# Performance work log

Measured on AMD Instinct MI355X. Metric: run time of the kernel, lower is better.

## Reference

```python
import jax, jax.numpy as jnp
import numpy as np

N = 50000      # nodes (single 'paper' node type)
E = 800000     # edges per etype
ET = 3         # edge types
L = 3          # GAT layers (1 + num_hidden=2)
H = 4          # heads
DH = 64        # per-head dim (n_hidden // n_heads)
NH = H * DH    # 256
NC = 16        # classes
NEG_SLOPE = 0.2


def setup_inputs() -> dict:
    key = jax.random.key(0)
    ks = jax.random.split(key, 8)
    x = jax.random.normal(ks[0], (N, NH), jnp.float32)
    src = jax.random.randint(ks[1], (ET, E), 0, N, jnp.int32)
    dst = jax.random.randint(ks[2], (ET, E), 0, N, jnp.int32)
    W = jax.random.normal(ks[3], (L, ET, NH, NH), jnp.float32) * 0.05
    attn_l = jax.random.normal(ks[4], (L, ET, H, DH), jnp.float32) * 0.05
    attn_r = jax.random.normal(ks[5], (L, ET, H, DH), jnp.float32) * 0.05
    bias = jnp.zeros((L, ET, NH), jnp.float32)
    lin_w = jax.random.normal(ks[6], (NH, NC), jnp.float32) * 0.05
    lin_b = jnp.zeros((NC,), jnp.float32)
    return {"x": x, "src": src, "dst": dst, "W": W, "attn_l": attn_l,
            "attn_r": attn_r, "bias": bias, "lin_w": lin_w, "lin_b": lin_b}


def _gat(h, W_e, al, ar, b, s, d):
    # h: [N, NH] -> z: [N, H, DH]
    z = (h @ W_e).reshape(N, H, DH)
    el = jnp.sum(z * al, axis=-1)             # [N, H]  (src-side score)
    er = jnp.sum(z * ar, axis=-1)             # [N, H]  (dst-side score)
    e = jax.nn.leaky_relu(el[s] + er[d], NEG_SLOPE)   # [E, H]
    # edge softmax over incoming edges of each dst node
    m = jax.ops.segment_max(e, d, num_segments=N)     # [N, H]
    a = jnp.exp(e - m[d])                              # [E, H]
    denom = jax.ops.segment_sum(a, d, num_segments=N) # [N, H]
    alpha = a / denom[d]                               # [E, H]
    # weighted aggregation of source features
    out = jax.ops.segment_sum(alpha[:, :, None] * z[s], d, num_segments=N)  # [N, H, DH]
    return out.reshape(N, NH) + b


def reference(x, src, dst, W, attn_l, attn_r, bias, lin_w, lin_b):
    h = x
    for l in range(L):
        acc = jnp.zeros((N, NH), h.dtype)
        for t in range(ET):  # HeteroGraphConv 'sum' aggregation across etypes
            acc = acc + _gat(h, W[l, t], attn_l[l, t], attn_r[l, t],
                             bias[l, t], src[t], dst[t])
        h = acc
        if l != L - 1:
            h = jax.nn.relu(h)  # dropout is identity in eval
    return h @ lin_w + lin_b    # [N, NC]
```

## Files before the change

kernel.cpp:

```cpp
#include <hip/hip_runtime.h>
#include <hip/hip_bf16.h>
#include <math.h>

#define N_NODES 50000
#define NEDGE 800000
#define NET 3
#define LAYERS 3
#define HEADS 4
#define DHEAD 64
#define NH 256
#define NC 16
#define NEG_SLOPE 0.2f
#define MPAD 50048

typedef __attribute__((ext_vector_type(8))) short short8;
typedef __attribute__((ext_vector_type(4))) float f32x4;
typedef __attribute__((ext_vector_type(8))) _Float16 half8;

#define GLDS16(gp, lp) \
  __builtin_amdgcn_global_load_lds((const __attribute__((address_space(1))) void*)(gp), \
                                   (__attribute__((address_space(3))) void*)(lp), 16, 0, 0)

__device__ inline unsigned short f2bf(float x) {
  unsigned u = __float_as_uint(x);
  unsigned r = (u + 0x7FFFu + ((u >> 16) & 1u)) >> 16;
  return (unsigned short)r;
}
__device__ inline float bf2f(unsigned short h) { return __uint_as_float(((unsigned)h) << 16); }

__global__ void split_transpose_W(const float* __restrict__ W,
                                  unsigned short* __restrict__ WhT,
                                  unsigned short* __restrict__ WlT) {
  int i = blockIdx.x * blockDim.x + threadIdx.x;
  if (i >= LAYERS * NET * NH * NH) return;
  int mat = i >> 16, rem = i & 65535;
  int n = rem >> 8, k = rem & 255;
  float v = W[(size_t)mat * 65536 + k * 256 + n];
  unsigned short hi = f2bf(v);
  unsigned short lo = f2bf(v - bf2f(hi));
  WhT[(size_t)mat * 65536 + n * 256 + k] = hi;
  WlT[(size_t)mat * 65536 + n * 256 + k] = lo;
}

__global__ void split_kernel(const float* __restrict__ in, unsigned short* __restrict__ hi,
                             unsigned short* __restrict__ lo) {
  int i = blockIdx.x * blockDim.x + threadIdx.x;
  if (i >= N_NODES * NH / 4) return;
  float4 v = ((const float4*)in)[i];
  ushort4 h, l;
  h.x = f2bf(v.x); l.x = f2bf(v.x - bf2f(h.x));
  h.y = f2bf(v.y); l.y = f2bf(v.y - bf2f(h.y));
  h.z = f2bf(v.z); l.z = f2bf(v.z - bf2f(h.z));
  h.w = f2bf(v.w); l.w = f2bf(v.w - bf2f(h.w));
  ((ushort4*)hi)[i] = h;
  ((ushort4*)lo)[i] = l;
}

__global__ __launch_bounds__(256) void gemm_split(const unsigned short* __restrict__ Ah,
                                                  const unsigned short* __restrict__ Al,
                                                  const unsigned short* __restrict__ BhT,
                                                  const unsigned short* __restrict__ BlT,
                                                  const float* __restrict__ al,
                                                  const float* __restrict__ ar,
                                                  _Float16* __restrict__ zh,
                                                  float* __restrict__ el,
                                                  float* __restrict__ er, int M) {
  __shared__ unsigned short lds[20480];
  unsigned short* sAh = lds;
  unsigned short* sAl = lds + 2048;
  unsigned short* sBh = lds + 4096;
  unsigned short* sBl = lds + 12288;

  int tid = threadIdx.x;
  int w = tid >> 6, lane = tid & 63;
  int r16 = lane & 15, rk = lane >> 4;
  int bm = blockIdx.x * 64;

  int arow = tid >> 2, acol = (tid & 3) * 8;
  const unsigned short* pAh = Ah + (size_t)(bm + arow) * 256 + acol;
  const unsigned short* pAl = Al + (size_t)(bm + arow) * 256 + acol;

  f32x4 acc[4][4];
#pragma unroll
  for (int m = 0; m < 4; m++)
#pragma unroll
    for (int n = 0; n < 4; n++) acc[m][n] = (f32x4){0.f, 0.f, 0.f, 0.f};

  char* aldsA = (char*)lds + (size_t)w * 1024;

#pragma unroll
  for (int k0 = 0; k0 < 8; k0++) {
    GLDS16(pAh + k0 * 32, aldsA);
    GLDS16(pAl + k0 * 32, (char*)sAl + (size_t)w * 1024);
#pragma unroll
    for (int i = 0; i < 4; i++) {
      int slot = tid + i * 256;
      int nrow = slot >> 2, kcol = (slot & 3) * 8;
      size_t go = (size_t)nrow * 256 + k0 * 32 + kcol;
      char* lb = (char*)sBh + ((size_t)w * 64 + (size_t)i * 256) * 16;
      char* lb2 = (char*)sBl + ((size_t)w * 64 + (size_t)i * 256) * 16;
      GLDS16(BhT + go, lb);
      GLDS16(BlT + go, lb2);
    }
    __syncthreads();

    short8 a_h[4], a_l[4], b_h[4], b_l[4];
#pragma unroll
    for (int m = 0; m < 4; m++) {
      a_h[m] = *(const short8*)&sAh[(m * 16 + r16) * 32 + rk * 8];
      a_l[m] = *(const short8*)&sAl[(m * 16 + r16) * 32 + rk * 8];
    }
#pragma unroll
    for (int n = 0; n < 4; n++) {
      int col = w * 64 + n * 16 + r16;
      b_h[n] = *(const short8*)&sBh[col * 32 + rk * 8];
      b_l[n] = *(const short8*)&sBl[col * 32 + rk * 8];
    }
#pragma unroll
    for (int m = 0; m < 4; m++)
#pragma unroll
      for (int n = 0; n < 4; n++) {
        acc[m][n] = __builtin_amdgcn_mfma_f32_16x16x32_bf16(a_h[m], b_h[n], acc[m][n], 0, 0, 0);
        acc[m][n] = __builtin_amdgcn_mfma_f32_16x16x32_bf16(a_h[m], b_l[n], acc[m][n], 0, 0, 0);
        acc[m][n] = __builtin_amdgcn_mfma_f32_16x16x32_bf16(a_l[m], b_h[n], acc[m][n], 0, 0, 0);
      }
    __syncthreads();
  }

#pragma unroll
  for (int m = 0; m < 4; m++) {
    int row0 = bm + m * 16 + rk * 4;
#pragma unroll
    for (int n = 0; n < 4; n++) {
      int col = w * 64 + n * 16 + r16;
#pragma unroll
      for (int r = 0; r < 4; r++) {
        int row = row0 + r;
        if (row < M) zh[(size_t)row * 256 + col] = (_Float16)acc[m][n][r];
      }
    }
  }

  float alv[4], arv[4];
#pragma unroll
  for (int n = 0; n < 4; n++) {
    alv[n] = al[w * 64 + n * 16 + r16];
    arv[n] = ar[w * 64 + n * 16 + r16];
  }
#pragma unroll
  for (int m = 0; m < 4; m++) {
#pragma unroll
    for (int r = 0; r < 4; r++) {
      float pl = 0.f, pr = 0.f;
#pragma unroll
      for (int n = 0; n < 4; n++) {
        float zv = acc[m][n][r];
        pl = fmaf(zv, alv[n], pl);
        pr = fmaf(zv, arv[n], pr);
      }
      pl += __shfl_xor(pl, 1, 64); pl += __shfl_xor(pl, 2, 64);
      pl += __shfl_xor(pl, 4, 64); pl += __shfl_xor(pl, 8, 64);
      pr += __shfl_xor(pr, 1, 64); pr += __shfl_xor(pr, 2, 64);
      pr += __shfl_xor(pr, 4, 64); pr += __shfl_xor(pr, 8, 64);
      int row = bm + m * 16 + rk * 4 + r;
      if (r16 == 0 && row < M) {
        el[row * HEADS + w] = pl;
        er[row * HEADS + w] = pr;
      }
    }
  }
}

__device__ inline float leaky(float v) { return v > 0.f ? v : NEG_SLOPE * v; }

__global__ void deg_kernel(const int* __restrict__ dst, int* __restrict__ deg) {
  int e = blockIdx.x * blockDim.x + threadIdx.x;
  if (e < NEDGE) atomicAdd(&deg[dst[e]], 1);
}

__global__ __launch_bounds__(1024) void scan_kernel(const int* __restrict__ deg,
                                                    int* __restrict__ rowptr) {
  __shared__ int wsum[16];
  __shared__ int carry_s;
  int tid = threadIdx.x;
  int lane = tid & 63, wv = tid >> 6;
  if (tid == 0) { carry_s = 0; rowptr[0] = 0; }
  __syncthreads();
  for (int base = 0; base < N_NODES; base += 1024) {
    int i = base + tid;
    int v = (i < N_NODES) ? deg[i] : 0;
    int x = v;
#pragma unroll
    for (int off = 1; off < 64; off <<= 1) {
      int y = __shfl_up(x, off, 64);
      if (lane >= off) x += y;
    }
    if (lane == 63) wsum[wv] = x;
    __syncthreads();
    if (wv == 0 && lane < 16) {
      int s = wsum[lane];
#pragma unroll
      for (int off = 1; off < 16; off <<= 1) {
        int y = __shfl_up(s, off, 16);
        if (lane >= off) s += y;
      }
      wsum[lane] = s;
    }
    __syncthreads();
    int waveoff = (wv > 0) ? wsum[wv - 1] : 0;
    int incl = x + waveoff + carry_s;
    if (i < N_NODES) rowptr[i + 1] = incl;
    __syncthreads();
    if (tid == 1023) carry_s = incl;
    __syncthreads();
  }
}

__global__ void scatter_kernel(const int* __restrict__ src, const int* __restrict__ dst,
                               int* __restrict__ cursor, int* __restrict__ col) {
  int e = blockIdx.x * blockDim.x + threadIdx.x;
  if (e < NEDGE) {
    int d = dst[e];
    int pos = atomicAdd(&cursor[d], 1);
    col[pos] = src[e];
  }
}

__global__ __launch_bounds__(256) void agg_kernel(const int* __restrict__ rowptr,
                                                  const int* __restrict__ col,
                                                  const float* __restrict__ el,
                                                  const float* __restrict__ er,
                                                  const _Float16* __restrict__ zh,
                                                  float* __restrict__ hout,
                                                  const float* __restrict__ b0,
                                                  const float* __restrict__ b1,
                                                  const float* __restrict__ b2,
                                                  int first, int addbias, int dorelu) {
  __shared__ float s_alpha[4][128][4];
  __shared__ int s_col[4][128];

  int wv = threadIdx.x >> 6, lane = threadIdx.x & 63;
  int n = blockIdx.x * 4 + wv;
  int rs = rowptr[n];
  int deg = rowptr[n + 1] - rs;

  int kk = lane & 15, hh = lane >> 4;
  float erh = er[n * HEADS + hh];
  int which = lane >> 5, lj = lane & 31, fh = lj >> 3;

  float sm = 0.f;
  float a0 = 0.f, a1 = 0.f, a2 = 0.f, a3 = 0.f;
  float a4 = 0.f, a5 = 0.f, a6 = 0.f, a7 = 0.f;

  for (int s0 = 0; s0 < deg; s0 += 128) {
    int segN = min(128, deg - s0);
    for (int c0 = 0; c0 < segN; c0 += 16) {
      if (c0 + kk < segN) {
        int s = col[rs + s0 + c0 + kk];
        float a = __expf(leaky(el[s * HEADS + hh] + erh));
        sm += a;
        s_alpha[wv][c0 + kk][hh] = a;
        if (hh == 0) s_col[wv][c0 + kk] = s;
      }
    }
    for (int k = which; k < segN; k += 2) {
      float a = s_alpha[wv][k][fh];
      int s = s_col[wv][k];
      half8 v = *(const half8*)&zh[(size_t)s * NH + lj * 8];
      a0 = fmaf(a, (float)v[0], a0);
      a1 = fmaf(a, (float)v[1], a1);
      a2 = fmaf(a, (float)v[2], a2);
      a3 = fmaf(a, (float)v[3], a3);
      a4 = fmaf(a, (float)v[4], a4);
      a5 = fmaf(a, (float)v[5], a5);
      a6 = fmaf(a, (float)v[6], a6);
      a7 = fmaf(a, (float)v[7], a7);
    }
  }

  sm += __shfl_xor(sm, 1, 64);
  sm += __shfl_xor(sm, 2, 64);
  sm += __shfl_xor(sm, 4, 64);
  sm += __shfl_xor(sm, 8, 64);
  float inv = (deg > 0) ? 1.f / sm : 0.f;
  float invb = __shfl(inv, fh * 16, 64);

  a0 += __shfl_xor(a0, 32, 64); a1 += __shfl_xor(a1, 32, 64);
  a2 += __shfl_xor(a2, 32, 64); a3 += __shfl_xor(a3, 32, 64);
  a4 += __shfl_xor(a4, 32, 64); a5 += __shfl_xor(a5, 32, 64);
  a6 += __shfl_xor(a6, 32, 64); a7 += __shfl_xor(a7, 32, 64);

  if (lane < 32) {
    int f0 = lj * 8;
    size_t oi = (size_t)n * NH + f0;
    float vo[8] = {a0 * invb, a1 * invb, a2 * invb, a3 * invb,
                   a4 * invb, a5 * invb, a6 * invb, a7 * invb};
    if (!first) {
      float4 p0 = *(const float4*)&hout[oi];
      float4 p1 = *(const float4*)&hout[oi + 4];
      vo[0] += p0.x; vo[1] += p0.y; vo[2] += p0.z; vo[3] += p0.w;
      vo[4] += p1.x; vo[5] += p1.y; vo[6] += p1.z; vo[7] += p1.w;
    }
    if (addbias) {
#pragma unroll
      for (int i = 0; i < 8; i++) vo[i] += b0[f0 + i] + b1[f0 + i] + b2[f0 + i];
    }
    if (dorelu) {
#pragma unroll
      for (int i = 0; i < 8; i++) vo[i] = fmaxf(vo[i], 0.f);
    }
    float4 o0 = {vo[0], vo[1], vo[2], vo[3]};
    float4 o1 = {vo[4], vo[5], vo[6], vo[7]};
    *(float4*)&hout[oi] = o0;
    *(float4*)&hout[oi + 4] = o1;
  }
}

__global__ __launch_bounds__(256) void linear_kernel(const float* __restrict__ h,
                                                     const float* __restrict__ w,
                                                     const float* __restrict__ b,
                                                     float* __restrict__ out) {
  __shared__ float part[16][17];
  int n = blockIdx.x;
  int t = threadIdx.x;
  int c = t & 15, p = t >> 4;
  float sum = 0.f;
#pragma unroll
  for (int q = 0; q < 16; q++) {
    int j = p * 16 + q;
    sum = fmaf(h[(size_t)n * NH + j], w[j * NC + c], sum);
  }
  part[p][c] = sum;
  __syncthreads();
  if (t < 16) {
    float s = 0.f;
#pragma unroll
    for (int p2 = 0; p2 < 16; p2++) s += part[p2][t];
    out[n * NC + t] = s + b[t];
  }
}

extern "C" void kernel_launch(void* const* d_in, const int* in_sizes, int n_in,
                              void* d_out, int out_size, void* d_ws, size_t ws_size,
                              hipStream_t stream) {
  const float* x      = (const float*)d_in[0];
  const int*   src    = (const int*)d_in[1];
  const int*   dst    = (const int*)d_in[2];
  const float* W      = (const float*)d_in[3];
  const float* attn_l = (const float*)d_in[4];
  const float* attn_r = (const float*)d_in[5];
  const float* bias   = (const float*)d_in[6];
  const float* lin_w  = (const float*)d_in[7];
  const float* lin_b  = (const float*)d_in[8];
  float* out = (float*)d_out;

  char* ws = (char*)d_ws;
  size_t off = 0;
  float* h  = (float*)(ws + off); off += (size_t)N_NODES * NH * 4;
  _Float16* zh = (_Float16*)(ws + off); off += (size_t)N_NODES * NH * 2;
  unsigned short* Ah = (unsigned short*)(ws + off); off += (size_t)MPAD * NH * 2;
  unsigned short* Al = (unsigned short*)(ws + off); off += (size_t)MPAD * NH * 2;
  unsigned short* WhT = (unsigned short*)(ws + off); off += (size_t)LAYERS * NET * NH * NH * 2;
  unsigned short* WlT = (unsigned short*)(ws + off); off += (size_t)LAYERS * NET * NH * NH * 2;
  float* el = (float*)(ws + off); off += (size_t)N_NODES * HEADS * 4;
  float* er = (float*)(ws + off); off += (size_t)N_NODES * HEADS * 4;
  int* rowptr[NET];
  for (int t = 0; t < NET; t++) { rowptr[t] = (int*)(ws + off); off += (size_t)(N_NODES + 1) * 4; }
  int* colA[NET];
  for (int t = 0; t < NET; t++) { colA[t] = (int*)(ws + off); off += (size_t)NEDGE * 4; }
  int* deg    = (int*)(ws + off); off += (size_t)N_NODES * 4;
  int* cursor = (int*)(ws + off); off += (size_t)N_NODES * 4;

  for (int t = 0; t < NET; t++) {
    const int* d_t = dst + (size_t)t * NEDGE;
    const int* s_t = src + (size_t)t * NEDGE;
    hipMemsetAsync(deg, 0, (size_t)N_NODES * 4, stream);
    deg_kernel<<<(NEDGE + 255) / 256, 256, 0, stream>>>(d_t, deg);
    scan_kernel<<<1, 1024, 0, stream>>>(deg, rowptr[t]);
    hipMemcpyAsync(cursor, rowptr[t], (size_t)N_NODES * 4, hipMemcpyDeviceToDevice, stream);
    scatter_kernel<<<(NEDGE + 255) / 256, 256, 0, stream>>>(s_t, d_t, cursor, colA[t]);
  }

  split_transpose_W<<<(LAYERS * NET * NH * NH + 255) / 256, 256, 0, stream>>>(W, WhT, WlT);

  for (int l = 0; l < LAYERS; l++) {
    const float* b0 = bias + (size_t)(l * NET + 0) * NH;
    const float* b1 = bias + (size_t)(l * NET + 1) * NH;
    const float* b2 = bias + (size_t)(l * NET + 2) * NH;

    const float* h_cur = (l == 0) ? x : h;
    split_kernel<<<(N_NODES * NH / 4 + 255) / 256, 256, 0, stream>>>(h_cur, Ah, Al);

    for (int t = 0; t < NET; t++) {
      const unsigned short* Bh = WhT + (size_t)(l * NET + t) * NH * NH;
      const unsigned short* Bl = WlT + (size_t)(l * NET + t) * NH * NH;
      const float* al = attn_l + (size_t)(l * NET + t) * HEADS * DHEAD;
      const float* ar = attn_r + (size_t)(l * NET + t) * HEADS * DHEAD;

      gemm_split<<<MPAD / 64, 256, 0, stream>>>(Ah, Al, Bh, Bl, al, ar, zh, el, er, N_NODES);
      agg_kernel<<<N_NODES / 4, 256, 0, stream>>>(rowptr[t], colA[t], el, er, zh, h,
                                                  b0, b1, b2,
                                                  t == 0, t == NET - 1,
                                                  (t == NET - 1) && (l != LAYERS - 1));
    }
  }
  linear_kernel<<<N_NODES, 256, 0, stream>>>(h, lin_w, lin_b, out);
}
```

Before: 1.583 ms.

## Fuse per-etype aggregations into one kernel and emit bf16 split inputs directly

```diff
diff --git a/kernel.cpp b/kernel.cpp
--- a/kernel.cpp
+++ b/kernel.cpp
@@ -217,102 +217,132 @@
 }
 
 __global__ void scatter_kernel(const int* __restrict__ src, const int* __restrict__ dst,
-                               int* __restrict__ cursor, int* __restrict__ col) {
+                               int* __restrict__ cursor, int* __restrict__ col, int rowoff) {
   int e = blockIdx.x * blockDim.x + threadIdx.x;
   if (e < NEDGE) {
     int d = dst[e];
     int pos = atomicAdd(&cursor[d], 1);
-    col[pos] = src[e];
-  }
-}
-
-__global__ __launch_bounds__(256) void agg_kernel(const int* __restrict__ rowptr,
-                                                  const int* __restrict__ col,
-                                                  const float* __restrict__ el,
-                                                  const float* __restrict__ er,
-                                                  const _Float16* __restrict__ zh,
-                                                  float* __restrict__ hout,
-                                                  const float* __restrict__ b0,
-                                                  const float* __restrict__ b1,
-                                                  const float* __restrict__ b2,
-                                                  int first, int addbias, int dorelu) {
+    col[pos] = src[e] + rowoff;
+  }
+}
+
+__global__ __launch_bounds__(256) void agg3_kernel(const int* __restrict__ rowptr,
+                                                   const int* __restrict__ col,
+                                                   const float* __restrict__ el,
+                                                   const float* __restrict__ er,
+                                                   const _Float16* __restrict__ zh,
+                                                   float* __restrict__ hout,
+                                                   unsigned short* __restrict__ Ah,
+                                                   unsigned short* __restrict__ Al,
+                                                   const float* __restrict__ b0,
+                                                   const float* __restrict__ b1,
+                                                   const float* __restrict__ b2,
+                                                   int final_layer) {
   __shared__ float s_alpha[4][128][4];
   __shared__ int s_col[4][128];
 
   int wv = threadIdx.x >> 6, lane = threadIdx.x & 63;
   int n = blockIdx.x * 4 + wv;
-  int rs = rowptr[n];
-  int deg = rowptr[n + 1] - rs;
-
   int kk = lane & 15, hh = lane >> 4;
-  float erh = er[n * HEADS + hh];
   int which = lane >> 5, lj = lane & 31, fh = lj >> 3;
 
-  float sm = 0.f;
-  float a0 = 0.f, a1 = 0.f, a2 = 0.f, a3 = 0.f;
-  float a4 = 0.f, a5 = 0.f, a6 = 0.f, a7 = 0.f;
-
-  for (int s0 = 0; s0 < deg; s0 += 128) {
-    int segN = min(128, deg - s0);
-    for (int c0 = 0; c0 < segN; c0 += 16) {
-      if (c0 + kk < segN) {
-        int s = col[rs + s0 + c0 + kk];
-        float a = __expf(leaky(el[s * HEADS + hh] + erh));
-        sm += a;
-        s_alpha[wv][c0 + kk][hh] = a;
-        if (hh == 0) s_col[wv][c0 + kk] = s;
-      }
-    }
-    for (int k = which; k < segN; k += 2) {
-      float a = s_alpha[wv][k][fh];
-      int s = s_col[wv][k];
-      half8 v = *(const half8*)&zh[(size_t)s * NH + lj * 8];
-      a0 = fmaf(a, (float)v[0], a0);
-      a1 = fmaf(a, (float)v[1], a1);
-      a2 = fmaf(a, (float)v[2], a2);
-      a3 = fmaf(a, (float)v[3], a3);
-      a4 = fmaf(a, (float)v[4], a4);
-      a5 = fmaf(a, (float)v[5], a5);
-      a6 = fmaf(a, (float)v[6], a6);
-      a7 = fmaf(a, (float)v[7], a7);
-    }
-  }
-
-  sm += __shfl_xor(sm, 1, 64);
-  sm += __shfl_xor(sm, 2, 64);
-  sm += __shfl_xor(sm, 4, 64);
-  sm += __shfl_xor(sm, 8, 64);
-  float inv = (deg > 0) ? 1.f / sm : 0.f;
-  float invb = __shfl(inv, fh * 16, 64);
-
-  a0 += __shfl_xor(a0, 32, 64); a1 += __shfl_xor(a1, 32, 64);
-  a2 += __shfl_xor(a2, 32, 64); a3 += __shfl_xor(a3, 32, 64);
-  a4 += __shfl_xor(a4, 32, 64); a5 += __shfl_xor(a5, 32, 64);
-  a6 += __shfl_xor(a6, 32, 64); a7 += __shfl_xor(a7, 32, 64);
+  float v0 = 0.f, v1 = 0.f, v2 = 0.f, v3 = 0.f;
+  float v4 = 0.f, v5 = 0.f, v6 = 0.f, v7 = 0.f;
+
+  for (int t = 0; t < NET; t++) {
+    int rs = rowptr[t * (N_NODES + 1) + n];
+    int deg = rowptr[t * (N_NODES + 1) + n + 1] - rs;
+    const int* colt = col + (size_t)t * NEDGE;
+    float erh = er[((size_t)t * N_NODES + n) * HEADS + hh];
+
+    float sm = 0.f;
+    float a0 = 0.f, a1 = 0.f, a2 = 0.f, a3 = 0.f;
+    float a4 = 0.f, a5 = 0.f, a6 = 0.f, a7 = 0.f;
+
+    for (int s0 = 0; s0 < deg; s0 += 128) {
+      int segN = min(128, deg - s0);
+      for (int c0 = 0; c0 < segN; c0 += 16) {
+        if (c0 + kk < segN) {
+          int row = colt[rs + s0 + c0 + kk];
+          float a = __expf(leaky(el[(size_t)row * HEADS + hh] + erh));
+          sm += a;
+          s_alpha[wv][c0 + kk][hh] = a;
+          if (hh == 0) s_col[wv][c0 + kk] = row;
+        }
+      }
+      int k = which;
+      for (; k + 2 < segN; k += 4) {
+        float aa = s_alpha[wv][k][fh];     int ra = s_col[wv][k];
+        float ab = s_alpha[wv][k + 2][fh]; int rb = s_col[wv][k + 2];
+        half8 va = *(const half8*)&zh[(size_t)ra * NH + lj * 8];
+        half8 vb = *(const half8*)&zh[(size_t)rb * NH + lj * 8];
+        a0 = fmaf(aa, (float)va[0], a0); a1 = fmaf(aa, (float)va[1], a1);
+        a2 = fmaf(aa, (float)va[2], a2); a3 = fmaf(aa, (float)va[3], a3);
+        a4 = fmaf(aa, (float)va[4], a4); a5 = fmaf(aa, (float)va[5], a5);
+        a6 = fmaf(aa, (float)va[6], a6); a7 = fmaf(aa, (float)va[7], a7);
+        a0 = fmaf(ab, (float)vb[0], a0); a1 = fmaf(ab, (float)vb[1], a1);
+        a2 = fmaf(ab, (float)vb[2], a2); a3 = fmaf(ab, (float)vb[3], a3);
+        a4 = fmaf(ab, (float)vb[4], a4); a5 = fmaf(ab, (float)vb[5], a5);
+        a6 = fmaf(ab, (float)vb[6], a6); a7 = fmaf(ab, (float)vb[7], a7);
+      }
+      for (; k < segN; k += 2) {
+        float aa = s_alpha[wv][k][fh];
+        int ra = s_col[wv][k];
+        half8 va = *(const half8*)&zh[(size_t)ra * NH + lj * 8];
+        a0 = fmaf(aa, (float)va[0], a0); a1 = fmaf(aa, (float)va[1], a1);
+        a2 = fmaf(aa, (float)va[2], a2); a3 = fmaf(aa, (float)va[3], a3);
+        a4 = fmaf(aa, (float)va[4], a4); a5 = fmaf(aa, (float)va[5], a5);
+        a6 = fmaf(aa, (float)va[6], a6); a7 = fmaf(aa, (float)va[7], a7);
+      }
+    }
+
+    sm += __shfl_xor(sm, 1, 64);
+    sm += __shfl_xor(sm, 2, 64);
+    sm += __shfl_xor(sm, 4, 64);
+    sm += __shfl_xor(sm, 8, 64);
+    float inv = (deg > 0) ? 1.f / sm : 0.f;
+    float invb = __shfl(inv, fh * 16, 64);
+
+    a0 += __shfl_xor(a0, 32, 64); a1 += __shfl_xor(a1, 32, 64);
+    a2 += __shfl_xor(a2, 32, 64); a3 += __shfl_xor(a3, 32, 64);
+    a4 += __shfl_xor(a4, 32, 64); a5 += __shfl_xor(a5, 32, 64);
+    a6 += __shfl_xor(a6, 32, 64); a7 += __shfl_xor(a7, 32, 64);
+
+    v0 = fmaf(a0, invb, v0); v1 = fmaf(a1, invb, v1);
+    v2 = fmaf(a2, invb, v2); v3 = fmaf(a3, invb, v3);
+    v4 = fmaf(a4, invb, v4); v5 = fmaf(a5, invb, v5);
+    v6 = fmaf(a6, invb, v6); v7 = fmaf(a7, invb, v7);
+  }
 
   if (lane < 32) {
     int f0 = lj * 8;
-    size_t oi = (size_t)n * NH + f0;
-    float vo[8] = {a0 * invb, a1 * invb, a2 * invb, a3 * invb,
-                   a4 * invb, a5 * invb, a6 * invb, a7 * invb};
-    if (!first) {
-      float4 p0 = *(const float4*)&hout[oi];
-      float4 p1 = *(const float4*)&hout[oi + 4];
-      vo[0] += p0.x; vo[1] += p0.y; vo[2] += p0.z; vo[3] += p0.w;
-      vo[4] += p1.x; vo[5] += p1.y; vo[6] += p1.z; vo[7] += p1.w;
-    }
-    if (addbias) {
-#pragma unroll
-      for (int i = 0; i < 8; i++) vo[i] += b0[f0 + i] + b1[f0 + i] + b2[f0 + i];
-    }
-    if (dorelu) {
+    float vo[8] = {v0, v1, v2, v3, v4, v5, v6, v7};
+#pragma unroll
+    for (int i = 0; i < 8; i++) vo[i] += b0[f0 + i] + b1[f0 + i] + b2[f0 + i];
+    if (final_layer) {
+      size_t oi = (size_t)n * NH + f0;
+      float4 o0 = {vo[0], vo[1], vo[2], vo[3]};
+      float4 o1 = {vo[4], vo[5], vo[6], vo[7]};
+      *(float4*)&hout[oi] = o0;
+      *(float4*)&hout[oi + 4] = o1;
+    } else {
+      ushort4 hi0, hi1, lo0, lo1;
 #pragma unroll
       for (int i = 0; i < 8; i++) vo[i] = fmaxf(vo[i], 0.f);
-    }
-    float4 o0 = {vo[0], vo[1], vo[2], vo[3]};
-    float4 o1 = {vo[4], vo[5], vo[6], vo[7]};
-    *(float4*)&hout[oi] = o0;
-    *(float4*)&hout[oi + 4] = o1;
+      hi0.x = f2bf(vo[0]); lo0.x = f2bf(vo[0] - bf2f(hi0.x));
+      hi0.y = f2bf(vo[1]); lo0.y = f2bf(vo[1] - bf2f(hi0.y));
+      hi0.z = f2bf(vo[2]); lo0.z = f2bf(vo[2] - bf2f(hi0.z));
+      hi0.w = f2bf(vo[3]); lo0.w = f2bf(vo[3] - bf2f(hi0.w));
+      hi1.x = f2bf(vo[4]); lo1.x = f2bf(vo[4] - bf2f(hi1.x));
+      hi1.y = f2bf(vo[5]); lo1.y = f2bf(vo[5] - bf2f(hi1.y));
+      hi1.z = f2bf(vo[6]); lo1.z = f2bf(vo[6] - bf2f(hi1.z));
+      hi1.w = f2bf(vo[7]); lo1.w = f2bf(vo[7] - bf2f(hi1.w));
+      size_t oi = (size_t)n * NH + f0;
+      *(ushort4*)&Ah[oi] = hi0;
+      *(ushort4*)&Ah[oi + 4] = hi1;
+      *(ushort4*)&Al[oi] = lo0;
+      *(ushort4*)&Al[oi + 4] = lo1;
+    }
   }
 }
 
@@ -356,53 +386,53 @@
 
   char* ws = (char*)d_ws;
   size_t off = 0;
-  float* h  = (float*)(ws + off); off += (size_t)N_NODES * NH * 4;
-  _Float16* zh = (_Float16*)(ws + off); off += (size_t)N_NODES * NH * 2;
+  _Float16* zh = (_Float16*)(ws + off); off += (size_t)NET * N_NODES * NH * 2;
   unsigned short* Ah = (unsigned short*)(ws + off); off += (size_t)MPAD * NH * 2;
   unsigned short* Al = (unsigned short*)(ws + off); off += (size_t)MPAD * NH * 2;
+  float* h = (float*)Ah;
   unsigned short* WhT = (unsigned short*)(ws + off); off += (size_t)LAYERS * NET * NH * NH * 2;
   unsigned short* WlT = (unsigned short*)(ws + off); off += (size_t)LAYERS * NET * NH * NH * 2;
-  float* el = (float*)(ws + off); off += (size_t)N_NODES * HEADS * 4;
-  float* er = (float*)(ws + off); off += (size_t)N_NODES * HEADS * 4;
-  int* rowptr[NET];
-  for (int t = 0; t < NET; t++) { rowptr[t] = (int*)(ws + off); off += (size_t)(N_NODES + 1) * 4; }
-  int* colA[NET];
-  for (int t = 0; t < NET; t++) { colA[t] = (int*)(ws + off); off += (size_t)NEDGE * 4; }
+  float* el = (float*)(ws + off); off += (size_t)NET * N_NODES * HEADS * 4;
+  float* er = (float*)(ws + off); off += (size_t)NET * N_NODES * HEADS * 4;
+  int* rowptr = (int*)(ws + off); off += (size_t)NET * (N_NODES + 1) * 4;
+  int* colA   = (int*)(ws + off); off += (size_t)NET * NEDGE * 4;
   int* deg    = (int*)(ws + off); off += (size_t)N_NODES * 4;
   int* cursor = (int*)(ws + off); off += (size_t)N_NODES * 4;
 
   for (int t = 0; t < NET; t++) {
     const int* d_t = dst + (size_t)t * NEDGE;
     const int* s_t = src + (size_t)t * NEDGE;
+    int* rp_t = rowptr + (size_t)t * (N_NODES + 1);
     hipMemsetAsync(deg, 0, (size_t)N_NODES * 4, stream);
     deg_kernel<<<(NEDGE + 255) / 256, 256, 0, stream>>>(d_t, deg);
-    scan_kernel<<<1, 1024, 0, stream>>>(deg, rowptr[t]);
-    hipMemcpyAsync(cursor, rowptr[t], (size_t)N_NODES * 4, hipMemcpyDeviceToDevice, stream);
-    scatter_kernel<<<(NEDGE + 255) / 256, 256, 0, stream>>>(s_t, d_t, cursor, colA[t]);
+    scan_kernel<<<1, 1024, 0, stream>>>(deg, rp_t);
+    hipMemcpyAsync(cursor, rp_t, (size_t)N_NODES * 4, hipMemcpyDeviceToDevice, stream);
+    scatter_kernel<<<(NEDGE + 255) / 256, 256, 0, stream>>>(s_t, d_t, cursor,
+                                                            colA + (size_t)t * NEDGE,
+                                                            t * N_NODES);
   }
 
   split_transpose_W<<<(LAYERS * NET * NH * NH + 255) / 256, 256, 0, stream>>>(W, WhT, WlT);
+
+  split_kernel<<<(N_NODES * NH / 4 + 255) / 256, 256, 0, stream>>>(x, Ah, Al);
 
   for (int l = 0; l < LAYERS; l++) {
     const float* b0 = bias + (size_t)(l * NET + 0) * NH;
     const float* b1 = bias + (size_t)(l * NET + 1) * NH;
     const float* b2 = bias + (size_t)(l * NET + 2) * NH;
-
-    const float* h_cur = (l == 0) ? x : h;
-    split_kernel<<<(N_NODES * NH / 4 + 255) / 256, 256, 0, stream>>>(h_cur, Ah, Al);
 
     for (int t = 0; t < NET; t++) {
       const unsigned short* Bh = WhT + (size_t)(l * NET + t) * NH * NH;
       const unsigned short* Bl = WlT + (size_t)(l * NET + t) * NH * NH;
       const float* al = attn_l + (size_t)(l * NET + t) * HEADS * DHEAD;
       const float* ar = attn_r + (size_t)(l * NET + t) * HEADS * DHEAD;
-
-      gemm_split<<<MPAD / 64, 256, 0, stream>>>(Ah, Al, Bh, Bl, al, ar, zh, el, er, N_NODES);
-      agg_kernel<<<N_NODES / 4, 256, 0, stream>>>(rowptr[t], colA[t], el, er, zh, h,
-                                                  b0, b1, b2,
-                                                  t == 0, t == NET - 1,
-                                                  (t == NET - 1) && (l != LAYERS - 1));
-    }
+      gemm_split<<<MPAD / 64, 256, 0, stream>>>(Ah, Al, Bh, Bl, al, ar,
+                                                zh + (size_t)t * N_NODES * NH,
+                                                el + (size_t)t * N_NODES * HEADS,
+                                                er + (size_t)t * N_NODES * HEADS, N_NODES);
+    }
+    agg3_kernel<<<N_NODES / 4, 256, 0, stream>>>(rowptr, colA, el, er, zh, h, Ah, Al,
+                                                 b0, b1, b2, l == LAYERS - 1);
   }
   linear_kernel<<<N_NODES, 256, 0, stream>>>(h, lin_w, lin_b, out);
 }
```

After: 1.479 ms. 1.07x faster.
